# Kernel tuning notes

Measured on AMD Instinct MI355X. Metric: run time of the kernel, lower is better.

The kernel has to match this reference:

```python
import jax, jax.numpy as jnp
import numpy as np

K = 3  # kernel size


def _bilinear_sample(x, px, py):
    """Bilinear sample x:[b,c,h,w] at pixel coords px,py:[b,t,h,w].
    Zeros padding, align_corners=True semantics (coords are raw pixel coords).
    Returns [b,c,t,h,w]."""
    b, c, h, w = x.shape
    x0 = jnp.floor(px)
    y0 = jnp.floor(py)
    wx1 = px - x0
    wx0 = 1.0 - wx1
    wy1 = py - y0
    wy0 = 1.0 - wy1
    xf = x.reshape(b, c, h * w)

    def gather(xi, yi):
        valid = (xi >= 0) & (xi <= w - 1) & (yi >= 0) & (yi <= h - 1)
        xi_c = jnp.clip(xi, 0, w - 1).astype(jnp.int32)
        yi_c = jnp.clip(yi, 0, h - 1).astype(jnp.int32)
        idx = (yi_c * w + xi_c).reshape(b, 1, -1)  # [b,1,t*h*w]
        v = jnp.take_along_axis(xf, idx, axis=2).reshape(b, c, *xi.shape[1:])
        return v * valid[:, None].astype(x.dtype)

    out = (gather(x0, y0) * (wx0 * wy0)[:, None]
           + gather(x0 + 1, y0) * (wx1 * wy0)[:, None]
           + gather(x0, y0 + 1) * (wx0 * wy1)[:, None]
           + gather(x0 + 1, y0 + 1) * (wx1 * wy1)[:, None])
    return out


def setup_inputs() -> dict:
    key = jax.random.key(0)
    k1, k2, k3 = jax.random.split(key, 3)
    b, c, h, w = 4, 64, 128, 128
    out_c = 64
    x = jax.random.normal(k1, (b, c, h, w), dtype=jnp.float32)
    offset = jax.random.normal(k2, (b, 2 * K * K, h, w), dtype=jnp.float32)
    weight = jax.random.normal(k3, (out_c, c, K, K), dtype=jnp.float32) * 0.05
    bias = jnp.zeros((out_c,), dtype=jnp.float32)
    return {"x": x, "offset": offset, "weight": weight, "bias": bias}


def reference(x, offset, weight, bias):
    b, c, h, w = x.shape
    kk = K * K
    # base integer grid (x along width, y along height)
    yy, xx = jnp.meshgrid(jnp.arange(h, dtype=x.dtype), jnp.arange(w, dtype=x.dtype), indexing='ij')
    off = offset.reshape(b, kk, 2, h, w)
    # grid_sample with align_corners=True inverts the module's normalization,
    # so effective sampling coords are simply base + offset in pixel space.
    px = xx[None, None] + off[:, :, 0]  # [b,kk,h,w]
    py = yy[None, None] + off[:, :, 1]
    sampled = _bilinear_sample(x, px, py)  # [b,c,kk,h,w]
    w2 = weight.reshape(weight.shape[0], c, kk)  # [o,c,kk]
    out = jnp.einsum('oct,bcthw->bohw', w2, sampled)
    return out + bias[None, :, None, None]
```

## Files before the change

### kernel.cpp

```cpp
#include <hip/hip_runtime.h>
#include <cstddef>

#define BH 4
#define CH 64
#define OH 64
#define HH 128
#define WW 128
#define KK 9
#define HW (HH * WW)

typedef __attribute__((ext_vector_type(8))) short short8;
typedef __attribute__((ext_vector_type(4))) float f32x4;
typedef __attribute__((ext_vector_type(2))) float f32x2;
typedef __attribute__((ext_vector_type(4))) unsigned int uint4v;

__device__ __forceinline__ unsigned short f2bf(float f) {
    unsigned u = __float_as_uint(f);
    u += 0x7fffu + ((u >> 16) & 1u);
    return (unsigned short)(u >> 16);
}

__device__ __forceinline__ f32x2 bf2x2(unsigned d) {
    f32x2 r;
    r.x = __uint_as_float(d << 16);
    r.y = __uint_as_float(d & 0xffff0000u);
    return r;
}
__device__ __forceinline__ unsigned pack_bf2(f32x2 v) {
    unsigned u0 = __float_as_uint(v.x);
    u0 += 0x7fffu + ((u0 >> 16) & 1u);
    unsigned u1 = __float_as_uint(v.y);
    u1 += 0x7fffu + ((u1 >> 16) & 1u);
    return __builtin_amdgcn_perm(u1, u0, 0x07060302);
}

__device__ __forceinline__ uint4v combine4(uint4v c00, uint4v c10, uint4v c01, uint4v c11,
                                           float w00, float w10, float w01, float w11) {
    f32x2 W00 = {w00, w00}, W10 = {w10, w10}, W01 = {w01, w01}, W11 = {w11, w11};
    uint4v r;
#pragma unroll
    for (int j = 0; j < 4; ++j) {
        f32x2 s = W00 * bf2x2(c00[j]) + W10 * bf2x2(c10[j])
                + W01 * bf2x2(c01[j]) + W11 * bf2x2(c11[j]);
        r[j] = pack_bf2(s);
    }
    return r;
}

__global__ __launch_bounds__(256) void dcl_transpose(const float* __restrict__ x,
                                                     unsigned short* __restrict__ xt) {
    __shared__ float tile[64][65];
    int chunk = blockIdx.x;
    int b = chunk >> 8;
    int hw0 = (chunk & 255) * 64;
    int tx = threadIdx.x;
    int ty = threadIdx.y;
    const float* xb = x + (size_t)b * CH * HW;
    for (int c = ty; c < 64; c += 4)
        tile[c][tx] = xb[(size_t)c * HW + hw0 + tx];
    __syncthreads();
    unsigned short* xtb = xt + ((size_t)b << 20);
    for (int i = ty; i < 64; i += 4)
        xtb[(size_t)(hw0 + i) * CH + tx] = f2bf(tile[tx][i]);
}

__global__ __launch_bounds__(256) void dcl_wpack(const float* __restrict__ wgt,
                                                 unsigned short* __restrict__ wtb) {
    int idx = blockIdx.x * 256 + threadIdx.x;
    int j  = idx & 7;
    int l  = (idx >> 3) & 63;
    int nt = (idx >> 9) & 3;
    int ks = idx >> 11;
    int k = ks * 32 + ((l >> 4) * 8) + j;
    int n = nt * 16 + (l & 15);
    int c = k & 63;
    int t = k >> 6;
    wtb[idx] = f2bf(wgt[(n * CH + c) * KK + t]);
}

#define WAVE_WORDS 1200

__global__ __launch_bounds__(256, 4) void dcl_main(
        const unsigned short* __restrict__ xt,
        const float* __restrict__ offset,
        const unsigned short* __restrict__ wtb,
        const float* __restrict__ bias,
        float* __restrict__ out) {
    __shared__ int smem[4 * WAVE_WORDS];
    int tid = threadIdx.x;
    int lane = tid & 63;
    int wave = tid >> 6;
    int* s_w = smem + wave * WAVE_WORDS;

    int P0 = blockIdx.x * 64 + wave * 16;
    int b = P0 >> 14;
    int rem0 = P0 & (HW - 1);
    int y = rem0 >> 7;
    int x0 = rem0 & 127;
    int m = lane & 15;
    int quad = lane >> 4;

    {
        int pm = lane & 15;
        int q = lane >> 4;
        float fx_base = (float)(x0 + pm);
        const float* offbase = offset + (((size_t)(b * 18)) << 14) + (rem0 + pm);
#pragma unroll
        for (int r = 0; r < 3; ++r) {
            int t = r * 4 + q;
            if (t < 9) {
                float ox = offbase[(size_t)(2 * t) << 14];
                float oy = offbase[(size_t)(2 * t + 1) << 14];
                float fx = fx_base + ox;
                float fy = (float)y + oy;
                float x0f = floorf(fx), y0f = floorf(fy);
                float wx1 = fx - x0f, wy1 = fy - y0f;
                float wx0 = 1.0f - wx1, wy0 = 1.0f - wy1;
                int ix0 = (int)x0f, iy0 = (int)y0f;
                int ix1 = ix0 + 1, iy1 = iy0 + 1;
                bool vx0 = (unsigned)ix0 < (unsigned)WW;
                bool vx1 = (unsigned)ix1 < (unsigned)WW;
                bool vy0 = (unsigned)iy0 < (unsigned)HH;
                bool vy1 = (unsigned)iy1 < (unsigned)HH;
                float w00 = (vx0 && vy0) ? wx0 * wy0 : 0.0f;
                float w10 = (vx1 && vy0) ? wx1 * wy0 : 0.0f;
                float w01 = (vx0 && vy1) ? wx0 * wy1 : 0.0f;
                float w11 = (vx1 && vy1) ? wx1 * wy1 : 0.0f;
                int cx0 = min(max(ix0, 0), WW - 1), cx1 = min(max(ix1, 0), WW - 1);
                int cy0 = min(max(iy0, 0), HH - 1), cy1 = min(max(iy1, 0), HH - 1);
                int base = b << 14;
                int o00 = (base + (cy0 << 7) + cx0) << 7;
                int o10 = (base + (cy0 << 7) + cx1) << 7;
                int o01 = (base + (cy1 << 7) + cx0) << 7;
                int o11 = (base + (cy1 << 7) + cx1) << 7;
                int* pp = s_w + t * 128 + pm;
                pp[0]   = __float_as_int(w00);
                pp[16]  = __float_as_int(w10);
                pp[32]  = __float_as_int(w01);
                pp[48]  = __float_as_int(w11);
                pp[64]  = o00;
                pp[80]  = o10;
                pp[96]  = o01;
                pp[112] = o11;
            }
        }
    }

    f32x4 acc[4];
#pragma unroll
    for (int i = 0; i < 4; ++i) acc[i] = (f32x4)(0.f);

    const short8* bfrags = (const short8*)wtb;
    const char* xtb = (const char*)xt;

#pragma unroll
    for (int t = 0; t < 9; ++t) {
        const int* pp = s_w + t * 128 + m;
        float w00 = __int_as_float(pp[0]);
        float w10 = __int_as_float(pp[16]);
        float w01 = __int_as_float(pp[32]);
        float w11 = __int_as_float(pp[48]);
        int qoff = quad * 16;
        int o00 = pp[64]  + qoff;
        int o10 = pp[80]  + qoff;
        int o01 = pp[96]  + qoff;
        int o11 = pp[112] + qoff;
        uint4v c00a = *(const uint4v*)(xtb + o00);
        uint4v c10a = *(const uint4v*)(xtb + o10);
        uint4v c01a = *(const uint4v*)(xtb + o01);
        uint4v c11a = *(const uint4v*)(xtb + o11);
        uint4v c00b = *(const uint4v*)(xtb + o00 + 64);
        uint4v c10b = *(const uint4v*)(xtb + o10 + 64);
        uint4v c01b = *(const uint4v*)(xtb + o01 + 64);
        uint4v c11b = *(const uint4v*)(xtb + o11 + 64);
        uint4v ra = combine4(c00a, c10a, c01a, c11a, w00, w10, w01, w11);
        uint4v rb = combine4(c00b, c10b, c01b, c11b, w00, w10, w01, w11);
        short8 aa = __builtin_bit_cast(short8, ra);
        short8 ab = __builtin_bit_cast(short8, rb);
        int ks = 2 * t;
#pragma unroll
        for (int nt = 0; nt < 4; ++nt)
            acc[nt] = __builtin_amdgcn_mfma_f32_16x16x32_bf16(
                aa, bfrags[(ks * 4 + nt) * 64 + lane], acc[nt], 0, 0, 0);
#pragma unroll
        for (int nt = 0; nt < 4; ++nt)
            acc[nt] = __builtin_amdgcn_mfma_f32_16x16x32_bf16(
                ab, bfrags[((ks + 1) * 4 + nt) * 64 + lane], acc[nt], 0, 0, 0);
    }

    float* o_w = (float*)s_w;
#pragma unroll
    for (int nt = 0; nt < 4; ++nt)
#pragma unroll
        for (int reg = 0; reg < 4; ++reg)
            o_w[(quad * 4 + reg) * 65 + nt * 16 + m] = acc[nt][reg];
    __syncthreads();

    int Pb0 = blockIdx.x * 64;
    int remb = Pb0 & (HW - 1);
#pragma unroll
    for (int j = tid; j < 64 * 64; j += 256) {
        int o = j >> 6;
        int p = j & 63;
        int w2 = p >> 4, mm = p & 15;
        float v = ((const float*)(smem + w2 * WAVE_WORDS))[mm * 65 + o] + bias[o];
        out[(((size_t)(b * OH + o)) << 14) + remb + p] = v;
    }
}

extern "C" void kernel_launch(void* const* d_in, const int* in_sizes, int n_in,
                              void* d_out, int out_size, void* d_ws, size_t ws_size,
                              hipStream_t stream) {
    const float* x      = (const float*)d_in[0];
    const float* offset = (const float*)d_in[1];
    const float* weight = (const float*)d_in[2];
    const float* bias   = (const float*)d_in[3];
    float* out = (float*)d_out;

    unsigned short* xt  = (unsigned short*)d_ws;
    unsigned short* wtb = (unsigned short*)((char*)d_ws + (size_t)BH * HW * CH * 2);

    dcl_transpose<<<(BH * HW) / 64, dim3(64, 4), 0, stream>>>(x, xt);
    dcl_wpack<<<(18 * 4 * 64 * 8) / 256, 256, 0, stream>>>(weight, wtb);
    dcl_main<<<(BH * HW) / 64, 256, 0, stream>>>(xt, offset, wtb, bias, out);
}
```

Measured before the change: 121.8 us.

## Split kernel taps across waves, merge prep kernels, vectorize transpose stores

```diff
diff --git a/kernel.cpp b/kernel.cpp
--- a/kernel.cpp
+++ b/kernel.cpp
@@ -13,13 +13,13 @@
 typedef __attribute__((ext_vector_type(4))) float f32x4;
 typedef __attribute__((ext_vector_type(2))) float f32x2;
 typedef __attribute__((ext_vector_type(4))) unsigned int uint4v;
+typedef __attribute__((ext_vector_type(4))) unsigned short ushort4v;
 
 __device__ __forceinline__ unsigned short f2bf(float f) {
     unsigned u = __float_as_uint(f);
     u += 0x7fffu + ((u >> 16) & 1u);
     return (unsigned short)(u >> 16);
 }
-
 __device__ __forceinline__ f32x2 bf2x2(unsigned d) {
     f32x2 r;
     r.x = __uint_as_float(d << 16);
@@ -33,7 +33,6 @@
     u1 += 0x7fffu + ((u1 >> 16) & 1u);
     return __builtin_amdgcn_perm(u1, u0, 0x07060302);
 }
-
 __device__ __forceinline__ uint4v combine4(uint4v c00, uint4v c10, uint4v c01, uint4v c11,
                                            float w00, float w10, float w01, float w11) {
     f32x2 W00 = {w00, w00}, W10 = {w10, w10}, W01 = {w01, w01}, W11 = {w11, w11};
@@ -47,52 +46,63 @@
     return r;
 }
 
-__global__ __launch_bounds__(256) void dcl_transpose(const float* __restrict__ x,
-                                                     unsigned short* __restrict__ xt) {
-    __shared__ float tile[64][65];
-    int chunk = blockIdx.x;
-    int b = chunk >> 8;
-    int hw0 = (chunk & 255) * 64;
-    int tx = threadIdx.x;
-    int ty = threadIdx.y;
-    const float* xb = x + (size_t)b * CH * HW;
-    for (int c = ty; c < 64; c += 4)
-        tile[c][tx] = xb[(size_t)c * HW + hw0 + tx];
-    __syncthreads();
-    unsigned short* xtb = xt + ((size_t)b << 20);
-    for (int i = ty; i < 64; i += 4)
-        xtb[(size_t)(hw0 + i) * CH + tx] = f2bf(tile[tx][i]);
-}
-
-__global__ __launch_bounds__(256) void dcl_wpack(const float* __restrict__ wgt,
-                                                 unsigned short* __restrict__ wtb) {
-    int idx = blockIdx.x * 256 + threadIdx.x;
-    int j  = idx & 7;
-    int l  = (idx >> 3) & 63;
-    int nt = (idx >> 9) & 3;
-    int ks = idx >> 11;
-    int k = ks * 32 + ((l >> 4) * 8) + j;
-    int n = nt * 16 + (l & 15);
-    int c = k & 63;
-    int t = k >> 6;
-    wtb[idx] = f2bf(wgt[(n * CH + c) * KK + t]);
-}
-
-#define WAVE_WORDS 1200
-
-__global__ __launch_bounds__(256, 4) void dcl_main(
+__global__ __launch_bounds__(256) void dcl_prep(const float* __restrict__ x,
+                                                const float* __restrict__ wgt,
+                                                unsigned short* __restrict__ xt,
+                                                unsigned short* __restrict__ wtb) {
+    if (blockIdx.x < 1024) {
+        __shared__ float tile[64][65];
+        int chunk = blockIdx.x;
+        int b = chunk >> 8;
+        int hw0 = (chunk & 255) * 64;
+        int tid = threadIdx.x;
+        int tx = tid & 63;
+        int ty = tid >> 6;
+        const float* xb = x + (size_t)b * CH * HW;
+#pragma unroll
+        for (int c = ty; c < 64; c += 4)
+            tile[c][tx] = xb[(size_t)c * HW + hw0 + tx];
+        __syncthreads();
+        unsigned short* xtb = xt + ((size_t)b << 20);
+        int c4 = (tid & 15) * 4;
+        int p0 = tid >> 4;
+#pragma unroll
+        for (int it = 0; it < 4; ++it) {
+            int pxl = p0 + it * 16;
+            ushort4v v = { f2bf(tile[c4 + 0][pxl]), f2bf(tile[c4 + 1][pxl]),
+                           f2bf(tile[c4 + 2][pxl]), f2bf(tile[c4 + 3][pxl]) };
+            *(ushort4v*)(xtb + (size_t)(hw0 + pxl) * CH + c4) = v;
+        }
+    } else {
+        int idx = (blockIdx.x - 1024) * 256 + threadIdx.x;
+        int j  = idx & 7;
+        int l  = (idx >> 3) & 63;
+        int nt = (idx >> 9) & 3;
+        int ks = idx >> 11;
+        int k = ks * 32 + ((l >> 4) * 8) + j;
+        int n = nt * 16 + (l & 15);
+        int c = k & 63;
+        int t = k >> 6;
+        wtb[idx] = f2bf(wgt[(n * CH + c) * KK + t]);
+    }
+}
+
+#define PREP_WORDS 1152
+#define OAREA_WORDS 1040
+#define SMEM_WORDS (2 * OAREA_WORDS)
+
+__global__ __launch_bounds__(128, 8) void dcl_main(
         const unsigned short* __restrict__ xt,
         const float* __restrict__ offset,
         const unsigned short* __restrict__ wtb,
         const float* __restrict__ bias,
         float* __restrict__ out) {
-    __shared__ int smem[4 * WAVE_WORDS];
+    __shared__ int smem[SMEM_WORDS];
     int tid = threadIdx.x;
     int lane = tid & 63;
     int wave = tid >> 6;
-    int* s_w = smem + wave * WAVE_WORDS;
-
-    int P0 = blockIdx.x * 64 + wave * 16;
+
+    int P0 = blockIdx.x * 16;
     int b = P0 >> 14;
     int rem0 = P0 & (HW - 1);
     int y = rem0 >> 7;
@@ -101,17 +111,16 @@
     int quad = lane >> 4;
 
     {
-        int pm = lane & 15;
-        int q = lane >> 4;
-        float fx_base = (float)(x0 + pm);
-        const float* offbase = offset + (((size_t)(b * 18)) << 14) + (rem0 + pm);
-#pragma unroll
-        for (int r = 0; r < 3; ++r) {
-            int t = r * 4 + q;
-            if (t < 9) {
+#pragma unroll
+        for (int rr = 0; rr < 2; ++rr) {
+            int e = tid + rr * 128;
+            if (e < 144) {
+                int t = e >> 4;
+                int pm = e & 15;
+                const float* offbase = offset + (((size_t)(b * 18)) << 14) + (rem0 + pm);
                 float ox = offbase[(size_t)(2 * t) << 14];
                 float oy = offbase[(size_t)(2 * t + 1) << 14];
-                float fx = fx_base + ox;
+                float fx = (float)(x0 + pm) + ox;
                 float fy = (float)y + oy;
                 float x0f = floorf(fx), y0f = floorf(fy);
                 float wx1 = fx - x0f, wy1 = fy - y0f;
@@ -133,7 +142,7 @@
                 int o10 = (base + (cy0 << 7) + cx1) << 7;
                 int o01 = (base + (cy1 << 7) + cx0) << 7;
                 int o11 = (base + (cy1 << 7) + cx1) << 7;
-                int* pp = s_w + t * 128 + pm;
+                int* pp = smem + t * 128 + pm;
                 pp[0]   = __float_as_int(w00);
                 pp[16]  = __float_as_int(w10);
                 pp[32]  = __float_as_int(w01);
@@ -145,6 +154,7 @@
             }
         }
     }
+    __syncthreads();
 
     f32x4 acc[4];
 #pragma unroll
@@ -153,42 +163,48 @@
     const short8* bfrags = (const short8*)wtb;
     const char* xtb = (const char*)xt;
 
-#pragma unroll
-    for (int t = 0; t < 9; ++t) {
-        const int* pp = s_w + t * 128 + m;
-        float w00 = __int_as_float(pp[0]);
-        float w10 = __int_as_float(pp[16]);
-        float w01 = __int_as_float(pp[32]);
-        float w11 = __int_as_float(pp[48]);
-        int qoff = quad * 16;
-        int o00 = pp[64]  + qoff;
-        int o10 = pp[80]  + qoff;
-        int o01 = pp[96]  + qoff;
-        int o11 = pp[112] + qoff;
-        uint4v c00a = *(const uint4v*)(xtb + o00);
-        uint4v c10a = *(const uint4v*)(xtb + o10);
-        uint4v c01a = *(const uint4v*)(xtb + o01);
-        uint4v c11a = *(const uint4v*)(xtb + o11);
-        uint4v c00b = *(const uint4v*)(xtb + o00 + 64);
-        uint4v c10b = *(const uint4v*)(xtb + o10 + 64);
-        uint4v c01b = *(const uint4v*)(xtb + o01 + 64);
-        uint4v c11b = *(const uint4v*)(xtb + o11 + 64);
-        uint4v ra = combine4(c00a, c10a, c01a, c11a, w00, w10, w01, w11);
-        uint4v rb = combine4(c00b, c10b, c01b, c11b, w00, w10, w01, w11);
-        short8 aa = __builtin_bit_cast(short8, ra);
-        short8 ab = __builtin_bit_cast(short8, rb);
-        int ks = 2 * t;
-#pragma unroll
-        for (int nt = 0; nt < 4; ++nt)
-            acc[nt] = __builtin_amdgcn_mfma_f32_16x16x32_bf16(
-                aa, bfrags[(ks * 4 + nt) * 64 + lane], acc[nt], 0, 0, 0);
-#pragma unroll
-        for (int nt = 0; nt < 4; ++nt)
-            acc[nt] = __builtin_amdgcn_mfma_f32_16x16x32_bf16(
-                ab, bfrags[((ks + 1) * 4 + nt) * 64 + lane], acc[nt], 0, 0, 0);
-    }
-
-    float* o_w = (float*)s_w;
+    int tbase = wave ? 5 : 0;
+    int tcnt  = wave ? 4 : 5;
+#pragma unroll
+    for (int i = 0; i < 5; ++i) {
+        if (i < tcnt) {
+            int t = tbase + i;
+            const int* pp = smem + t * 128 + m;
+            float w00 = __int_as_float(pp[0]);
+            float w10 = __int_as_float(pp[16]);
+            float w01 = __int_as_float(pp[32]);
+            float w11 = __int_as_float(pp[48]);
+            int qoff = quad * 16;
+            int o00 = pp[64]  + qoff;
+            int o10 = pp[80]  + qoff;
+            int o01 = pp[96]  + qoff;
+            int o11 = pp[112] + qoff;
+            uint4v c00a = *(const uint4v*)(xtb + o00);
+            uint4v c10a = *(const uint4v*)(xtb + o10);
+            uint4v c01a = *(const uint4v*)(xtb + o01);
+            uint4v c11a = *(const uint4v*)(xtb + o11);
+            uint4v c00b = *(const uint4v*)(xtb + o00 + 64);
+            uint4v c10b = *(const uint4v*)(xtb + o10 + 64);
+            uint4v c01b = *(const uint4v*)(xtb + o01 + 64);
+            uint4v c11b = *(const uint4v*)(xtb + o11 + 64);
+            uint4v ra = combine4(c00a, c10a, c01a, c11a, w00, w10, w01, w11);
+            uint4v rb = combine4(c00b, c10b, c01b, c11b, w00, w10, w01, w11);
+            short8 aa = __builtin_bit_cast(short8, ra);
+            short8 ab = __builtin_bit_cast(short8, rb);
+            int ks = 2 * t;
+#pragma unroll
+            for (int nt = 0; nt < 4; ++nt)
+                acc[nt] = __builtin_amdgcn_mfma_f32_16x16x32_bf16(
+                    aa, bfrags[(ks * 4 + nt) * 64 + lane], acc[nt], 0, 0, 0);
+#pragma unroll
+            for (int nt = 0; nt < 4; ++nt)
+                acc[nt] = __builtin_amdgcn_mfma_f32_16x16x32_bf16(
+                    ab, bfrags[((ks + 1) * 4 + nt) * 64 + lane], acc[nt], 0, 0, 0);
+        }
+    }
+
+    __syncthreads();
+    float* o_w = (float*)(smem + wave * OAREA_WORDS);
 #pragma unroll
     for (int nt = 0; nt < 4; ++nt)
 #pragma unroll
@@ -196,15 +212,14 @@
             o_w[(quad * 4 + reg) * 65 + nt * 16 + m] = acc[nt][reg];
     __syncthreads();
 
-    int Pb0 = blockIdx.x * 64;
-    int remb = Pb0 & (HW - 1);
-#pragma unroll
-    for (int j = tid; j < 64 * 64; j += 256) {
-        int o = j >> 6;
-        int p = j & 63;
-        int w2 = p >> 4, mm = p & 15;
-        float v = ((const float*)(smem + w2 * WAVE_WORDS))[mm * 65 + o] + bias[o];
-        out[(((size_t)(b * OH + o)) << 14) + remb + p] = v;
+    const float* o0 = (const float*)smem;
+    const float* o1 = (const float*)(smem + OAREA_WORDS);
+#pragma unroll
+    for (int j = tid; j < 16 * 64; j += 128) {
+        int o = j >> 4;
+        int p = j & 15;
+        float v = o0[p * 65 + o] + o1[p * 65 + o] + bias[o];
+        out[(((size_t)(b * OH + o)) << 14) + rem0 + p] = v;
     }
 }
 
@@ -220,7 +235,6 @@
     unsigned short* xt  = (unsigned short*)d_ws;
     unsigned short* wtb = (unsigned short*)((char*)d_ws + (size_t)BH * HW * CH * 2);
 
-    dcl_transpose<<<(BH * HW) / 64, dim3(64, 4), 0, stream>>>(x, xt);
-    dcl_wpack<<<(18 * 4 * 64 * 8) / 256, 256, 0, stream>>>(weight, wtb);
-    dcl_main<<<(BH * HW) / 64, 256, 0, stream>>>(xt, offset, wtb, bias, out);
-}
+    dcl_prep<<<1024 + 144, 256, 0, stream>>>(x, weight, xt, wtb);
+    dcl_main<<<(BH * HW) / 16, 128, 0, stream>>>(xt, offset, wtb, bias, out);
+}
```

Result: faster. 119.2 us (-2.1%).
